# Optimization experiments

Hardware: AMD Instinct MI355X
Metric: run time of the kernel (lower is better)

Reference implementation:

```python
import jax, jax.numpy as jnp
import numpy as np
import math

K = 7
PAD = 3

def _aniso_kernel(k, sigma_h, sigma_v, angle):
    ax = np.linspace(-(k // 2), k // 2, k, dtype=np.float32)
    xx, yy = np.meshgrid(ax, ax, indexing='ij')
    x_rot = xx * math.cos(angle) + yy * math.sin(angle)
    y_rot = -xx * math.sin(angle) + yy * math.cos(angle)
    ker = np.exp(-(x_rot ** 2 / (2 * sigma_h ** 2) + y_rot ** 2 / (2 * sigma_v ** 2)))
    ker = ker / (ker.sum() + 1e-8)
    return jnp.asarray(ker, dtype=jnp.float32)  # (k,k)

BASE_H = _aniso_kernel(K, 2.5, 1.0, 0.0)
BASE_V = _aniso_kernel(K, 2.5, 1.0, math.pi / 2)

def setup_inputs() -> dict:
    key = jax.random.key(0)
    k1, k2, k3, k4 = jax.random.split(key, 4)
    B, C, H, W, MID = 8, 256, 128, 128, 16
    x = jax.random.normal(k1, (B, C, H, W), dtype=jnp.float32)
    angle_map = jax.random.uniform(k2, (B, H, W), dtype=jnp.float32) * math.pi
    w_reduce = jax.random.normal(k3, (MID, C), dtype=jnp.float32) * 0.05
    w_expand = jax.random.normal(k4, (C, MID), dtype=jnp.float32) * 0.05
    return {"x": x, "angle_map": angle_map, "w_reduce": w_reduce, "w_expand": w_expand}

def reference(x, angle_map, w_reduce, w_expand):
    B, C, H, W = x.shape
    # 1x1 conv reduce: (B,C,H,W) x (mid,C) -> (B,mid,H,W)
    x_low = jnp.einsum('bchw,mc->bmhw', x, w_reduce)
    # per-pixel blend weights
    w_h = jnp.cos(angle_map) ** 2                      # (B,H,W)
    combined = (w_h[..., None, None] * BASE_H
                + (1.0 - w_h)[..., None, None] * BASE_V)  # (B,H,W,k,k)
    combined = combined.reshape(B, H, W, K * K)
    # reflect pad and extract kxk patches (stride 1 -> output spatial == H,W)
    x_pad = jnp.pad(x_low, ((0, 0), (0, 0), (PAD, PAD), (PAD, PAD)), mode='reflect')
    patches = jnp.stack(
        [x_pad[:, :, i:i + H, j:j + W] for i in range(K) for j in range(K)],
        axis=-1)                                       # (B,mid,H,W,k*k)
    out_low = jnp.einsum('bmhwk,bhwk->bmhw', patches, combined)
    out_low = jnp.nan_to_num(out_low)
    out = jnp.einsum('bmhw,cm->bchw', out_low, w_expand)
    return jnp.nan_to_num(out)
```

## Files before the change

kernel.cpp:

```cpp
#include <hip/hip_runtime.h>

#define Bn   8
#define Cn   256
#define MIDn 16
#define Hn   128
#define Wn   128
#define HWn  (Hn * Wn)

__global__ __launch_bounds__(256, 4) void reduce_k(const float2* __restrict__ x2,
                                                   const float* __restrict__ wr,
                                                   float2* __restrict__ xlow2) {
    __shared__ float2 comb[4][MIDn][64];

    const int tid = threadIdx.x;
    const int p2  = tid & 63;
    const int wv  = tid >> 6;
    const int b   = blockIdx.y;
    const int p0  = blockIdx.x * 64;

    const int c0 = __builtin_amdgcn_readfirstlane(wv << 6);

    const float2* xb = x2 + ((size_t)b * Cn + c0) * (HWn / 2) + p0 + p2;

    float2 acc[MIDn];
#pragma unroll
    for (int m = 0; m < MIDn; ++m) acc[m] = make_float2(0.f, 0.f);

#pragma unroll 8
    for (int c = 0; c < 64; ++c) {
        const float2 v = xb[(size_t)c * (HWn / 2)];
        const float* w = wr + (c0 + c);
#pragma unroll
        for (int m = 0; m < MIDn; ++m) {
            const float wm = w[m * Cn];
            acc[m].x = fmaf(v.x, wm, acc[m].x);
            acc[m].y = fmaf(v.y, wm, acc[m].y);
        }
    }

#pragma unroll
    for (int m = 0; m < MIDn; ++m) comb[wv][m][p2] = acc[m];
    __syncthreads();

    float2* ob = xlow2 + (size_t)b * MIDn * (HWn / 2) + p0;
#pragma unroll
    for (int k = 0; k < 4; ++k) {
        const int idx = k * 256 + tid;
        const int m   = idx >> 6;
        const int q   = idx & 63;
        const float2 s0 = comb[0][m][q];
        const float2 s1 = comb[1][m][q];
        const float2 s2 = comb[2][m][q];
        const float2 s3 = comb[3][m][q];
        float2 s;
        s.x = (s0.x + s1.x) + (s2.x + s3.x);
        s.y = (s0.y + s1.y) + (s2.y + s3.y);
        ob[(size_t)m * (HWn / 2) + q] = s;
    }
}

#define TW 32
#define TH 4
#define HR (TH + 6)
#define WR (TW + 6)
#define NPX (TH * TW)
#define NSTRIP (MIDn * WR)

__device__ __forceinline__ int reflect_i(int i, int n) {
    return i < 0 ? -i : (i >= n ? 2 * n - 2 - i : i);
}

__global__ __launch_bounds__(256, 4) void conv_expand_k(const float* __restrict__ xlow,
                                                        const float* __restrict__ ang,
                                                        const float* __restrict__ we,
                                                        float2* __restrict__ out2) {
    __shared__ float tile[MIDn][HR][WR];
    __shared__ float low[MIDn][NPX];

    const int tid = threadIdx.x;
    const int b   = blockIdx.y;
    const int rem = blockIdx.x;
    const int th0 = (rem >> 2) * TH;
    const int tw0 = (rem & 3) * TW;

    const int px = tid & (NPX - 1);
    const int mh = tid >> 7;
    const int pr = px >> 5;
    const int pc = px & 31;
    const float a = ang[(size_t)b * HWn + (th0 + pr) * Wn + (tw0 + pc)];

    const float fu0 = 0.48675226f, fu1 = 0.72614904f, fu2 = 0.92311635f;
    const float fv0 = 0.011108997f, fv1 = 0.13533528f, fv2 = 0.60653066f;

    const float* pb = xlow + (size_t)b * MIDn * HWn;
    for (int idx = tid; idx < MIDn * HR * WR; idx += 256) {
        const int m  = idx / (HR * WR);
        const int r2 = idx - m * (HR * WR);
        const int r  = r2 / WR;
        const int cc = r2 - r * WR;
        const int gr = reflect_i(th0 + r - 3, Hn);
        const int gc = reflect_i(tw0 + cc - 3, Wn);
        tile[m][r][cc] = pb[(size_t)m * HWn + gr * Wn + gc];
    }
    __syncthreads();

    float oA[8], oB[8], oC[8];
    int mA, cA, mB, cB, mC, cC;
    bool hasC;
    {
        {
            const int s = tid;
            mA = s / WR; cA = s - mA * WR;
            float t[HR];
#pragma unroll
            for (int r = 0; r < HR; ++r) t[r] = tile[mA][r][cA];
#pragma unroll
            for (int r = 0; r < TH; ++r) {
                const float p06 = t[r] + t[r + 6];
                const float p15 = t[r + 1] + t[r + 5];
                const float p24 = t[r + 2] + t[r + 4];
                const float p3  = t[r + 3];
                oA[r]     = fmaf(fu0, p06, fmaf(fu1, p15, fmaf(fu2, p24, p3)));
                oA[4 + r] = fmaf(fv0, p06, fmaf(fv1, p15, fmaf(fv2, p24, p3)));
            }
        }
        {
            const int s = tid + 256;
            mB = s / WR; cB = s - mB * WR;
            float t[HR];
#pragma unroll
            for (int r = 0; r < HR; ++r) t[r] = tile[mB][r][cB];
#pragma unroll
            for (int r = 0; r < TH; ++r) {
                const float p06 = t[r] + t[r + 6];
                const float p15 = t[r + 1] + t[r + 5];
                const float p24 = t[r + 2] + t[r + 4];
                const float p3  = t[r + 3];
                oB[r]     = fmaf(fu0, p06, fmaf(fu1, p15, fmaf(fu2, p24, p3)));
                oB[4 + r] = fmaf(fv0, p06, fmaf(fv1, p15, fmaf(fv2, p24, p3)));
            }
        }
        hasC = (tid + 512) < NSTRIP;
        {
            const int s = hasC ? (tid + 512) : tid;
            mC = s / WR; cC = s - mC * WR;
            float t[HR];
#pragma unroll
            for (int r = 0; r < HR; ++r) t[r] = tile[mC][r][cC];
#pragma unroll
            for (int r = 0; r < TH; ++r) {
                const float p06 = t[r] + t[r + 6];
                const float p15 = t[r + 1] + t[r + 5];
                const float p24 = t[r + 2] + t[r + 4];
                const float p3  = t[r + 3];
                oC[r]     = fmaf(fu0, p06, fmaf(fu1, p15, fmaf(fu2, p24, p3)));
                oC[4 + r] = fmaf(fv0, p06, fmaf(fv1, p15, fmaf(fv2, p24, p3)));
            }
        }
    }
    __syncthreads();

#pragma unroll
    for (int r = 0; r < TH; ++r) {
        tile[mA][r][cA]     = oA[r];
        tile[mA][4 + r][cA] = oA[4 + r];
        tile[mB][r][cB]     = oB[r];
        tile[mB][4 + r][cB] = oB[4 + r];
    }
    if (hasC) {
#pragma unroll
        for (int r = 0; r < TH; ++r) {
            tile[mC][r][cC]     = oC[r];
            tile[mC][4 + r][cC] = oC[4 + r];
        }
    }
    __syncthreads();

    {
        const float ch = cosf(a);
        const float wh = ch * ch;
        const float su = 1.f + 2.f * (0.48675226f + 0.72614904f + 0.92311635f);
        const float sv = 1.f + 2.f * (0.011108997f + 0.13533528f + 0.60653066f);
        const float inv = 1.f / (su * sv + 1e-8f);
        const float aH = wh * inv;
        const float aV = (1.f - wh) * inv;

        const int m0 = mh * 8;
#pragma unroll
        for (int mm = 0; mm < 8; ++mm) {
            const int m = m0 + mm;
            const float h06 = tile[m][pr][pc] + tile[m][pr][pc + 6];
            const float h15 = tile[m][pr][pc + 1] + tile[m][pr][pc + 5];
            const float h24 = tile[m][pr][pc + 2] + tile[m][pr][pc + 4];
            const float accH = fmaf(fv0, h06, fmaf(fv1, h15, fmaf(fv2, h24, tile[m][pr][pc + 3])));
            const float g06 = tile[m][4 + pr][pc] + tile[m][4 + pr][pc + 6];
            const float g15 = tile[m][4 + pr][pc + 1] + tile[m][4 + pr][pc + 5];
            const float g24 = tile[m][4 + pr][pc + 2] + tile[m][4 + pr][pc + 4];
            const float accV = fmaf(fu0, g06, fmaf(fu1, g15, fmaf(fu2, g24, tile[m][4 + pr][pc + 3])));
            low[m][px] = fmaf(aH, accH, aV * accV);
        }
    }
    __syncthreads();

    const int p2 = tid & 63;
    const int c0 = __builtin_amdgcn_readfirstlane((tid >> 6) << 6);

    const float2* low2 = (const float2*)low;
    float2 lw[MIDn];
#pragma unroll
    for (int m = 0; m < MIDn; ++m) lw[m] = low2[m * 64 + p2];

    const int gh  = th0 + (p2 >> 4);
    const int gw2 = (tw0 >> 1) + (p2 & 15);
    float2* ob = out2 + ((size_t)b * Cn + c0) * (HWn / 2) + gh * (Wn / 2) + gw2;

#pragma unroll 4
    for (int ci = 0; ci < 64; ++ci) {
        const float* w = we + (size_t)(c0 + ci) * MIDn;
        float2 o = make_float2(0.f, 0.f);
#pragma unroll
        for (int m = 0; m < MIDn; ++m) {
            o.x = fmaf(w[m], lw[m].x, o.x);
            o.y = fmaf(w[m], lw[m].y, o.y);
        }
        ob[(size_t)ci * (HWn / 2)] = o;
    }
}

extern "C" void kernel_launch(void* const* d_in, const int* in_sizes, int n_in,
                              void* d_out, int out_size, void* d_ws, size_t ws_size,
                              hipStream_t stream) {
    const float* x   = (const float*)d_in[0];
    const float* ang = (const float*)d_in[1];
    const float* wr  = (const float*)d_in[2];
    const float* we  = (const float*)d_in[3];
    float*       out = (float*)d_out;

    float* xlow = (float*)d_ws;

    reduce_k<<<dim3((HWn / 2) / 64, Bn), dim3(256), 0, stream>>>(
        (const float2*)x, wr, (float2*)xlow);
    conv_expand_k<<<dim3(128, Bn), dim3(256), 0, stream>>>(xlow, ang, we, (float2*)out);
}
```

Measured before the change: 257.9 us.

## Keep blended conv results in registers and expand per pixel without LDS round-trip

Each thread now computes all 16 mid channels of the blended conv for its own pixel, keeps them in registers, and expands straight to 128 output channels with scalar stores. This removes the low[] shared-memory buffer, one barrier and the LDS reload. It also raises the launch-bounds occupancy hint to 6. In exchange the two halves of the block redundantly compute the same 16-channel conv per pixel, and output stores become 4-byte instead of 8-byte.

After: 268.8 us. 4.2% more time.

```diff
diff --git a/kernel.cpp b/kernel.cpp
--- a/kernel.cpp
+++ b/kernel.cpp
@@ -70,12 +70,11 @@
     return i < 0 ? -i : (i >= n ? 2 * n - 2 - i : i);
 }
 
-__global__ __launch_bounds__(256, 4) void conv_expand_k(const float* __restrict__ xlow,
+__global__ __launch_bounds__(256, 6) void conv_expand_k(const float* __restrict__ xlow,
                                                         const float* __restrict__ ang,
                                                         const float* __restrict__ we,
-                                                        float2* __restrict__ out2) {
+                                                        float* __restrict__ out) {
     __shared__ float tile[MIDn][HR][WR];
-    __shared__ float low[MIDn][NPX];
 
     const int tid = threadIdx.x;
     const int b   = blockIdx.y;
@@ -84,9 +83,9 @@
     const int tw0 = (rem & 3) * TW;
 
     const int px = tid & (NPX - 1);
-    const int mh = tid >> 7;
     const int pr = px >> 5;
     const int pc = px & 31;
+
     const float a = ang[(size_t)b * HWn + (th0 + pr) * Wn + (tw0 + pc)];
 
     const float fu0 = 0.48675226f, fu1 = 0.72614904f, fu2 = 0.92311635f;
@@ -176,6 +175,7 @@
     }
     __syncthreads();
 
+    float lowr[MIDn];
     {
         const float ch = cosf(a);
         const float wh = ch * ch;
@@ -185,10 +185,8 @@
         const float aH = wh * inv;
         const float aV = (1.f - wh) * inv;
 
-        const int m0 = mh * 8;
-#pragma unroll
-        for (int mm = 0; mm < 8; ++mm) {
-            const int m = m0 + mm;
+#pragma unroll
+        for (int m = 0; m < MIDn; ++m) {
             const float h06 = tile[m][pr][pc] + tile[m][pr][pc + 6];
             const float h15 = tile[m][pr][pc + 1] + tile[m][pr][pc + 5];
             const float h24 = tile[m][pr][pc + 2] + tile[m][pr][pc + 4];
@@ -197,33 +195,20 @@
             const float g15 = tile[m][4 + pr][pc + 1] + tile[m][4 + pr][pc + 5];
             const float g24 = tile[m][4 + pr][pc + 2] + tile[m][4 + pr][pc + 4];
             const float accV = fmaf(fu0, g06, fmaf(fu1, g15, fmaf(fu2, g24, tile[m][4 + pr][pc + 3])));
-            low[m][px] = fmaf(aH, accH, aV * accV);
-        }
-    }
-    __syncthreads();
-
-    const int p2 = tid & 63;
-    const int c0 = __builtin_amdgcn_readfirstlane((tid >> 6) << 6);
-
-    const float2* low2 = (const float2*)low;
-    float2 lw[MIDn];
-#pragma unroll
-    for (int m = 0; m < MIDn; ++m) lw[m] = low2[m * 64 + p2];
-
-    const int gh  = th0 + (p2 >> 4);
-    const int gw2 = (tw0 >> 1) + (p2 & 15);
-    float2* ob = out2 + ((size_t)b * Cn + c0) * (HWn / 2) + gh * (Wn / 2) + gw2;
-
+            lowr[m] = fmaf(aH, accH, aV * accV);
+        }
+    }
+
+    const int ch0 = __builtin_amdgcn_readfirstlane((tid >> 7) << 7);
+
+    float* ob = out + ((size_t)b * Cn + ch0) * HWn + (th0 + pr) * Wn + (tw0 + pc);
 #pragma unroll 4
-    for (int ci = 0; ci < 64; ++ci) {
-        const float* w = we + (size_t)(c0 + ci) * MIDn;
-        float2 o = make_float2(0.f, 0.f);
-#pragma unroll
-        for (int m = 0; m < MIDn; ++m) {
-            o.x = fmaf(w[m], lw[m].x, o.x);
-            o.y = fmaf(w[m], lw[m].y, o.y);
-        }
-        ob[(size_t)ci * (HWn / 2)] = o;
+    for (int ci = 0; ci < 128; ++ci) {
+        const float* w = we + (size_t)(ch0 + ci) * MIDn;
+        float o = 0.f;
+#pragma unroll
+        for (int m = 0; m < MIDn; ++m) o = fmaf(w[m], lowr[m], o);
+        ob[(size_t)ci * HWn] = o;
     }
 }
 
@@ -240,5 +225,5 @@
 
     reduce_k<<<dim3((HWn / 2) / 64, Bn), dim3(256), 0, stream>>>(
         (const float2*)x, wr, (float2*)xlow);
-    conv_expand_k<<<dim3(128, Bn), dim3(256), 0, stream>>>(xlow, ang, we, (float2*)out);
-}
+    conv_expand_k<<<dim3(128, Bn), dim3(256), 0, stream>>>(xlow, ang, we, out);
+}
```
